# Kernel tuning notes

Hardware: AMD Instinct MI355X
Metric: run time of the kernel (lower is better)

The kernel has to match this reference:

```python
import jax, jax.numpy as jnp
import numpy as np
from jax import lax

B = 16
C_IN = 103      # image_channels / conv_inputs (spectral bands)
H = W = 9       # patch size
C_CONV = 256    # conv_outputs == primary_unit_size (in_size of routing)
N_PRIM = 32     # num_primary_units (in_units, contracted dim)
N_OUT = 103     # num_output_units
D_OUT = 16      # output_unit_size
N_ITER = 3
REC = H * W * C_IN          # 8343
H1 = int(REC * 2 / 3)       # 5562
H2 = int(REC * 3 / 2)       # 12514


def squash(s, axis):
    # torch: mag_sq/(1+mag_sq) * s/mag, reduced over `axis`
    mag_sq = jnp.sum(s * s, axis=axis, keepdims=True)
    mag = jnp.sqrt(mag_sq)
    return mag_sq / (1.0 + mag_sq) * (s / mag)


def setup_inputs() -> dict:
    key = jax.random.key(0)
    ks = jax.random.split(key, 10)
    x = jax.random.normal(ks[0], (B, C_IN, H, W), jnp.float32)
    conv_w = 0.05 * jax.random.normal(ks[1], (C_CONV, C_IN, 3, 3), jnp.float32)
    conv_b = jnp.zeros((C_CONV,), jnp.float32)
    # torch: nn.Parameter(torch.randn(1, in_size, out_units, out_size, in_units)); drop leading 1
    W_caps = jax.random.normal(ks[2], (C_CONV, N_OUT, D_OUT, N_PRIM), jnp.float32)
    fc1_w = 0.02 * jax.random.normal(ks[3], (N_OUT * D_OUT, H1), jnp.float32)
    fc1_b = jnp.zeros((H1,), jnp.float32)
    fc2_w = 0.02 * jax.random.normal(ks[4], (H1, H2), jnp.float32)
    fc2_b = jnp.zeros((H2,), jnp.float32)
    fc3_w = 0.02 * jax.random.normal(ks[5], (H2, REC), jnp.float32)
    fc3_b = jnp.zeros((REC,), jnp.float32)
    return {"x": x, "conv_w": conv_w, "conv_b": conv_b, "W_caps": W_caps,
            "fc1_w": fc1_w, "fc1_b": fc1_b, "fc2_w": fc2_w, "fc2_b": fc2_b,
            "fc3_w": fc3_w, "fc3_b": fc3_b}


def reference(x, conv_w, conv_b, W_caps, fc1_w, fc1_b, fc2_w, fc2_b, fc3_w, fc3_b):
    # ConvLayer: 3x3 valid conv + relu -> [B, C_CONV, 7, 7]
    h = lax.conv_general_dilated(x, conv_w, (1, 1), 'VALID',
                                 dimension_numbers=('NCHW', 'OIHW', 'NCHW'))
    h = jax.nn.relu(h + conv_b[None, :, None, None])

    # PrimaryCapsuleLayer: N_PRIM identical AdaptiveAvgPool2d(1) units
    p = h.mean(axis=(2, 3))                                   # [B, C_CONV]
    u = jnp.broadcast_to(p[:, None, :], (B, N_PRIM, C_CONV))  # [B, N_PRIM, C_CONV]
    u = squash(u, axis=2)

    # CapsuleLayer dynamic routing
    xt = u.transpose(0, 2, 1)                                 # [B, C_CONV, N_PRIM]
    # u_hat[b,c,j,o] = sum_i W[c,j,o,i] * xt[b,c,i]
    u_hat = jnp.einsum('cjoi,bci->bcjo', W_caps, xt)          # [B, C_CONV, N_OUT, D_OUT]

    b_ij = jnp.ones((1, C_CONV, N_OUT, 1), u_hat.dtype)
    v_j = None
    for _ in range(N_ITER):
        c_ij = jax.nn.softmax(b_ij, axis=1)                   # softmax over in_size
        s_j = jnp.sum(c_ij * u_hat, axis=1, keepdims=True)    # [B, 1, N_OUT, D_OUT]
        v_j = squash(s_j, axis=2)                             # torch squashes over out_units dim
        agree = jnp.sum(u_hat * v_j, axis=3, keepdims=True)   # [B, C_CONV, N_OUT, 1]
        b_ij = b_ij + agree.mean(axis=0, keepdims=True)

    v = v_j[:, 0]                                             # [B, N_OUT, D_OUT]
    # band_attention = ||v_j||_2 over out_size, shape [B, N_OUT, 1, 1] (torch)
    ba = jnp.linalg.norm(v, axis=-1, keepdims=True)[..., None]

    # ReconstructionLayer on attention-weighted capsules
    f = (v * ba[..., 0]).reshape(B, -1)                       # [B, N_OUT*D_OUT]
    f = f @ fc1_w + fc1_b
    f = f @ fc2_w + fc2_b
    f = f @ fc3_w + fc3_b
    recon = f.reshape(B, C_IN, H, W)
    return ba, recon
```

## Files before the change

kernel.cpp:

```cpp
#include <hip/hip_runtime.h>
#include <math.h>

#define BATCH 16
#define CIN 103
#define CCONV 256
#define NOUT 103
#define DOUT 16
#define RECSZ 8343
#define H1SZ 5562
#define H2SZ 12514

#define WS_P      0
#define WS_SQ     4096
#define WS_WSUM   8192
#define WS_BB     430080
#define WS_S      456448
#define WS_FACTOR 482816
#define WS_F0     483072
#define WS_F1     509440
#define WS_F2     598432

__global__ __launch_bounds__(256) void init_k(float* __restrict__ f1, const float* __restrict__ b1,
                                              float* __restrict__ f2, const float* __restrict__ b2,
                                              float* __restrict__ f3, const float* __restrict__ b3,
                                              float* __restrict__ bb) {
    int i = blockIdx.x * 256 + threadIdx.x;
    if (i < 16 * H1SZ) { f1[i] = b1[i % H1SZ]; return; }
    i -= 16 * H1SZ;
    if (i < 16 * H2SZ) { f2[i] = b2[i % H2SZ]; return; }
    i -= 16 * H2SZ;
    if (i < 16 * RECSZ) { f3[i] = b3[i % RECSZ]; return; }
    i -= 16 * RECSZ;
    if (i < 103 * 256) bb[i] = 1.0f;
}

__global__ __launch_bounds__(256) void conv_pool_k(const float* __restrict__ x,
                                                   const float* __restrict__ w,
                                                   const float* __restrict__ cb,
                                                   float* __restrict__ p) {
    int b = blockIdx.x >> 6;
    int cob = (blockIdx.x & 63) << 2;
    __shared__ float xs[CIN * 81];
    int t = threadIdx.x;
    for (int i = t; i < CIN * 81; i += 256) xs[i] = x[(size_t)b * CIN * 81 + i];
    __syncthreads();
    int wave = t >> 6, lane = t & 63;
    int co = cob + wave;
    co = __builtin_amdgcn_readfirstlane(co);
    int pos = lane < 49 ? lane : 0;
    int oh = pos / 7, ow = pos % 7;
    const float* wp = w + (size_t)co * CIN * 9;
    const float* xp = xs + oh * 9 + ow;
    float acc = 0.f;
    for (int ci = 0; ci < CIN; ++ci) {
#pragma unroll
        for (int kh = 0; kh < 3; ++kh)
#pragma unroll
            for (int kw = 0; kw < 3; ++kw)
                acc = fmaf(xp[ci * 81 + kh * 9 + kw], wp[ci * 9 + kh * 3 + kw], acc);
    }
    acc += cb[co];
    acc = fmaxf(acc, 0.f);
    if (lane >= 49) acc = 0.f;
#pragma unroll
    for (int off = 32; off; off >>= 1) acc += __shfl_down(acc, off);
    if (lane == 0) p[b * 256 + co] = acc * (1.0f / 49.0f);
}

__global__ __launch_bounds__(256) void squash_p_k(const float* __restrict__ p, float* __restrict__ sq) {
    int b = blockIdx.x, c = threadIdx.x;
    float v = p[b * 256 + c];
    float ss = v * v;
#pragma unroll
    for (int off = 32; off; off >>= 1) ss += __shfl_down(ss, off);
    __shared__ float red[4];
    if ((c & 63) == 0) red[c >> 6] = ss;
    __syncthreads();
    float ms = red[0] + red[1] + red[2] + red[3];
    float mag = sqrtf(ms);
    sq[b * 256 + c] = v * mag / (1.f + ms);
}

__global__ __launch_bounds__(256) void wsum_k(const float* __restrict__ Wc, float* __restrict__ wsum) {
    int idx = blockIdx.x * 256 + threadIdx.x;
    const float4* p4 = (const float4*)(Wc + (size_t)idx * 32);
    float s = 0.f;
#pragma unroll
    for (int q = 0; q < 8; ++q) { float4 v = p4[q]; s += v.x + v.y + v.z + v.w; }
    wsum[idx] = s;
}

__global__ __launch_bounds__(256) void route_s_k(const float* __restrict__ sq,
                                                 const float* __restrict__ wsum,
                                                 const float* __restrict__ bb,
                                                 float* __restrict__ s_out) {
    int j = blockIdx.x;
    int t = threadIdx.x;
    __shared__ float sqst[4096];
    __shared__ float wls[4096];
    __shared__ float cc[256];
    __shared__ float red[8];
    float bv = bb[j * 256 + t];
    for (int i = t; i < 4096; i += 256) {
        sqst[i] = sq[((i & 15) << 8) + (i >> 4)];
        wls[i] = wsum[(size_t)(i >> 4) * (103 * 16) + j * 16 + (i & 15)];
    }
    int wave = t >> 6, lane = t & 63;
    float m = bv;
#pragma unroll
    for (int off = 32; off; off >>= 1) m = fmaxf(m, __shfl_down(m, off));
    if (lane == 0) red[wave] = m;
    __syncthreads();
    m = fmaxf(fmaxf(red[0], red[1]), fmaxf(red[2], red[3]));
    float e = expf(bv - m);
    float ssum = e;
#pragma unroll
    for (int off = 32; off; off >>= 1) ssum += __shfl_down(ssum, off);
    if (lane == 0) red[4 + wave] = ssum;
    __syncthreads();
    ssum = red[4] + red[5] + red[6] + red[7];
    cc[t] = e / ssum;
    __syncthreads();
    for (int i = t; i < 4096; i += 256) sqst[i] *= cc[i >> 4];
    __syncthreads();
    int b = t >> 4, o = t & 15;
    float acc = 0.f;
    for (int c = 0; c < 256; ++c)
        acc = fmaf(sqst[c * 16 + b], wls[c * 16 + o], acc);
    s_out[((size_t)b * 103 + j) * 16 + o] = acc;
}

__global__ __launch_bounds__(256) void factor_k(const float* __restrict__ s, float* __restrict__ factor) {
    int t = threadIdx.x;
    int b = t >> 4, o = t & 15;
    float ms = 0.f;
    for (int j = 0; j < 103; ++j) {
        float v = s[((size_t)b * 103 + j) * 16 + o];
        ms = fmaf(v, v, ms);
    }
    factor[t] = sqrtf(ms) / (1.f + ms);
}

__global__ __launch_bounds__(256) void route_upd_k(const float* __restrict__ sq,
                                                   const float* __restrict__ wsum,
                                                   const float* __restrict__ s,
                                                   const float* __restrict__ factor,
                                                   float* __restrict__ bb) {
    int j = blockIdx.x;
    int t = threadIdx.x;
    __shared__ float vs[256];
    {
        int b = t >> 4, o = t & 15;
        vs[t] = s[((size_t)b * 103 + j) * 16 + o] * factor[t];
    }
    __syncthreads();
    const float4* wp = (const float4*)(wsum + ((size_t)t * 103 + j) * 16);
    float4 w0 = wp[0], w1 = wp[1], w2 = wp[2], w3 = wp[3];
    float wv[16] = {w0.x, w0.y, w0.z, w0.w, w1.x, w1.y, w1.z, w1.w,
                    w2.x, w2.y, w2.z, w2.w, w3.x, w3.y, w3.z, w3.w};
    float acc = 0.f;
#pragma unroll
    for (int b = 0; b < 16; ++b) {
        float d = 0.f;
#pragma unroll
        for (int o = 0; o < 16; ++o) d = fmaf(wv[o], vs[b * 16 + o], d);
        acc = fmaf(sq[b * 256 + t], d, acc);
    }
    bb[j * 256 + t] += acc * (1.0f / 16.0f);
}

__global__ __launch_bounds__(256) void final_v_k(const float* __restrict__ s,
                                                 const float* __restrict__ factor,
                                                 float* __restrict__ out_ba,
                                                 float* __restrict__ f0) {
    int idx = blockIdx.x * 256 + threadIdx.x;
    if (idx >= 16 * 103) return;
    int b = idx / 103;
    const float4* sp = (const float4*)(s + (size_t)idx * 16);
    float4 s0 = sp[0], s1 = sp[1], s2 = sp[2], s3 = sp[3];
    float sv[16] = {s0.x, s0.y, s0.z, s0.w, s1.x, s1.y, s1.z, s1.w,
                    s2.x, s2.y, s2.z, s2.w, s3.x, s3.y, s3.z, s3.w};
    float v[16];
    float nrm2 = 0.f;
#pragma unroll
    for (int o = 0; o < 16; ++o) {
        v[o] = sv[o] * factor[b * 16 + o];
        nrm2 = fmaf(v[o], v[o], nrm2);
    }
    float ba = sqrtf(nrm2);
    out_ba[idx] = ba;
    float4* fp = (float4*)(f0 + (size_t)idx * 16);
    float4 r0 = {v[0] * ba, v[1] * ba, v[2] * ba, v[3] * ba};
    float4 r1 = {v[4] * ba, v[5] * ba, v[6] * ba, v[7] * ba};
    float4 r2 = {v[8] * ba, v[9] * ba, v[10] * ba, v[11] * ba};
    float4 r3 = {v[12] * ba, v[13] * ba, v[14] * ba, v[15] * ba};
    fp[0] = r0; fp[1] = r1; fp[2] = r2; fp[3] = r3;
}

template <bool V2>
__global__ __launch_bounds__(256) void fc_k(const float* __restrict__ in,
                                            const float* __restrict__ w,
                                            float* __restrict__ out,
                                            int K, int N, int kchunk) {
    extern __shared__ float sact[];
    const int k0 = blockIdx.y * kchunk;
    int nk = K - k0; if (nk > kchunk) nk = kchunk;
    for (int i = threadIdx.x; i < (nk << 4); i += 256)
        sact[i] = in[(i & 15) * K + k0 + (i >> 4)];
    __syncthreads();

    const int c0 = blockIdx.x * 512 + (threadIdx.x << 1);
    const bool st0 = c0 < N;
    const bool st1 = c0 + 1 < N;
    const int c = st0 ? c0 : 0;
    const int off1 = st1 ? 1 : 0;
    const float* wp = w + (size_t)k0 * N + c;
    const size_t Ns = (size_t)N;

    float a0[16], a1[16];
#pragma unroll
    for (int b = 0; b < 16; ++b) { a0[b] = 0.f; a1[b] = 0.f; }

    int k = 0;
    for (; k + 4 <= nk; k += 4) {
        float w00, w01, w10, w11, w20, w21, w30, w31;
        if (V2) {
            float2 q0 = *(const float2*)(wp);
            float2 q1 = *(const float2*)(wp + Ns);
            float2 q2 = *(const float2*)(wp + 2 * Ns);
            float2 q3 = *(const float2*)(wp + 3 * Ns);
            w00 = q0.x; w01 = q0.y; w10 = q1.x; w11 = q1.y;
            w20 = q2.x; w21 = q2.y; w30 = q3.x; w31 = q3.y;
        } else {
            w00 = wp[0];          w01 = wp[off1];
            w10 = wp[Ns];         w11 = wp[Ns + off1];
            w20 = wp[2 * Ns];     w21 = wp[2 * Ns + off1];
            w30 = wp[3 * Ns];     w31 = wp[3 * Ns + off1];
        }
        wp += 4 * Ns;
        const float* s0 = sact + (k << 4);
#pragma unroll
        for (int b = 0; b < 16; ++b) {
            float v0 = s0[b], v1 = s0[16 + b], v2 = s0[32 + b], v3 = s0[48 + b];
            a0[b] = fmaf(v0, w00, a0[b]);
            a1[b] = fmaf(v0, w01, a1[b]);
            a0[b] = fmaf(v1, w10, a0[b]);
            a1[b] = fmaf(v1, w11, a1[b]);
            a0[b] = fmaf(v2, w20, a0[b]);
            a1[b] = fmaf(v2, w21, a1[b]);
            a0[b] = fmaf(v3, w30, a0[b]);
            a1[b] = fmaf(v3, w31, a1[b]);
        }
    }
    for (; k < nk; ++k) {
        float wv0, wv1;
        if (V2) { float2 q = *(const float2*)(wp); wv0 = q.x; wv1 = q.y; }
        else    { wv0 = wp[0]; wv1 = wp[off1]; }
        wp += Ns;
        const float* s0 = sact + (k << 4);
#pragma unroll
        for (int b = 0; b < 16; ++b) {
            a0[b] = fmaf(s0[b], wv0, a0[b]);
            a1[b] = fmaf(s0[b], wv1, a1[b]);
        }
    }
    if (st0) {
#pragma unroll
        for (int b = 0; b < 16; ++b) atomicAdd(&out[b * Ns + c], a0[b]);
    }
    if (st1) {
#pragma unroll
        for (int b = 0; b < 16; ++b) atomicAdd(&out[b * Ns + c + 1], a1[b]);
    }
}

extern "C" void kernel_launch(void* const* d_in, const int* in_sizes, int n_in,
                              void* d_out, int out_size, void* d_ws, size_t ws_size,
                              hipStream_t stream) {
    const float* x      = (const float*)d_in[0];
    const float* conv_w = (const float*)d_in[1];
    const float* conv_b = (const float*)d_in[2];
    const float* W_caps = (const float*)d_in[3];
    const float* fc1_w  = (const float*)d_in[4];
    const float* fc1_b  = (const float*)d_in[5];
    const float* fc2_w  = (const float*)d_in[6];
    const float* fc2_b  = (const float*)d_in[7];
    const float* fc3_w  = (const float*)d_in[8];
    const float* fc3_b  = (const float*)d_in[9];
    float* out = (float*)d_out;
    float* ws  = (float*)d_ws;

    float* p      = ws + WS_P;
    float* sq     = ws + WS_SQ;
    float* wsum   = ws + WS_WSUM;
    float* bb     = ws + WS_BB;
    float* s      = ws + WS_S;
    float* factor = ws + WS_FACTOR;
    float* f0     = ws + WS_F0;
    float* f1     = ws + WS_F1;
    float* f2     = ws + WS_F2;
    float* ba_out = out;
    float* recon  = out + 1648;

    init_k<<<1755, 256, 0, stream>>>(f1, fc1_b, f2, fc2_b, recon, fc3_b, bb);

    conv_pool_k<<<1024, 256, 0, stream>>>(x, conv_w, conv_b, p);
    squash_p_k<<<16, 256, 0, stream>>>(p, sq);
    wsum_k<<<1648, 256, 0, stream>>>(W_caps, wsum);

    for (int it = 0; it < 3; ++it) {
        route_s_k<<<103, 256, 0, stream>>>(sq, wsum, bb, s);
        factor_k<<<1, 256, 0, stream>>>(s, factor);
        if (it < 2)
            route_upd_k<<<103, 256, 0, stream>>>(sq, wsum, s, factor, bb);
    }
    final_v_k<<<7, 256, 0, stream>>>(s, factor, ba_out, f0);

    fc_k<true><<<dim3(11, 46), 256, 36 * 16 * 4, stream>>>(f0, fc1_w, f1, 1648, H1SZ, 36);
    fc_k<true><<<dim3(25, 20), 256, 279 * 16 * 4, stream>>>(f1, fc2_w, f2, H1SZ, H2SZ, 279);
    fc_k<false><<<dim3(17, 30), 256, 418 * 16 * 4, stream>>>(f2, fc3_w, recon, H2SZ, RECSZ, 418);
}
```

Measured before the change: 1.071 ms.

## Replace atomic split-K with partial buffers, transposed activations, and double-buffered weight loads

The three FC layers now write per-K-chunk partial sums to workspace, and separate reduction kernels sum them and add the bias. This removes the atomicAdd traffic and the bias-init kernel. Activations are kept in a k-major transposed layout, so shared-memory staging reads contiguously. The inner loop loads weights in groups of 8 rows with register double buffering to hide global load latency. The grids are re-split to use more K chunks and occupancy is raised with launch bounds, at the cost of extra partial-buffer memory traffic and three more launches.

```diff
diff --git a/kernel.cpp b/kernel.cpp
--- a/kernel.cpp
+++ b/kernel.cpp
@@ -19,18 +19,12 @@
 #define WS_F0     483072
 #define WS_F1     509440
 #define WS_F2     598432
-
-__global__ __launch_bounds__(256) void init_k(float* __restrict__ f1, const float* __restrict__ b1,
-                                              float* __restrict__ f2, const float* __restrict__ b2,
-                                              float* __restrict__ f3, const float* __restrict__ b3,
-                                              float* __restrict__ bb) {
+#define WS_PART1  798656
+#define WS_PART2  4536320
+#define WS_PART3  12345056
+
+__global__ __launch_bounds__(256) void init_bb_k(float* __restrict__ bb) {
     int i = blockIdx.x * 256 + threadIdx.x;
-    if (i < 16 * H1SZ) { f1[i] = b1[i % H1SZ]; return; }
-    i -= 16 * H1SZ;
-    if (i < 16 * H2SZ) { f2[i] = b2[i % H2SZ]; return; }
-    i -= 16 * H2SZ;
-    if (i < 16 * RECSZ) { f3[i] = b3[i % RECSZ]; return; }
-    i -= 16 * RECSZ;
     if (i < 103 * 256) bb[i] = 1.0f;
 }
 
@@ -172,10 +166,11 @@
 __global__ __launch_bounds__(256) void final_v_k(const float* __restrict__ s,
                                                  const float* __restrict__ factor,
                                                  float* __restrict__ out_ba,
-                                                 float* __restrict__ f0) {
+                                                 float* __restrict__ f0t) {
     int idx = blockIdx.x * 256 + threadIdx.x;
     if (idx >= 16 * 103) return;
     int b = idx / 103;
+    int j = idx - b * 103;
     const float4* sp = (const float4*)(s + (size_t)idx * 16);
     float4 s0 = sp[0], s1 = sp[1], s2 = sp[2], s3 = sp[3];
     float sv[16] = {s0.x, s0.y, s0.z, s0.w, s1.x, s1.y, s1.z, s1.w,
@@ -189,24 +184,53 @@
     }
     float ba = sqrtf(nrm2);
     out_ba[idx] = ba;
-    float4* fp = (float4*)(f0 + (size_t)idx * 16);
-    float4 r0 = {v[0] * ba, v[1] * ba, v[2] * ba, v[3] * ba};
-    float4 r1 = {v[4] * ba, v[5] * ba, v[6] * ba, v[7] * ba};
-    float4 r2 = {v[8] * ba, v[9] * ba, v[10] * ba, v[11] * ba};
-    float4 r3 = {v[12] * ba, v[13] * ba, v[14] * ba, v[15] * ba};
-    fp[0] = r0; fp[1] = r1; fp[2] = r2; fp[3] = r3;
-}
-
-template <bool V2>
-__global__ __launch_bounds__(256) void fc_k(const float* __restrict__ in,
-                                            const float* __restrict__ w,
-                                            float* __restrict__ out,
-                                            int K, int N, int kchunk) {
+    float* fp = f0t + ((size_t)j << 8) + b;
+#pragma unroll
+    for (int o = 0; o < 16; ++o) fp[o << 4] = v[o] * ba;
+}
+
+#define FC_LOADG(b0, b1, kk)                                          \
+    {                                                                 \
+        const float* wq = wp + (size_t)(kk) * Ns;                     \
+        if (V2) {                                                     \
+            _Pragma("unroll")                                         \
+            for (int r = 0; r < 8; ++r) {                             \
+                float2 q = *(const float2*)(wq + (size_t)r * Ns);     \
+                b0[r] = q.x; b1[r] = q.y;                             \
+            }                                                         \
+        } else {                                                      \
+            _Pragma("unroll")                                         \
+            for (int r = 0; r < 8; ++r) {                             \
+                b0[r] = wq[(size_t)r * Ns];                           \
+                b1[r] = wq[(size_t)r * Ns + off1];                    \
+            }                                                         \
+        }                                                             \
+    }
+
+#define FC_COMP(b0, b1, kk)                                           \
+    {                                                                 \
+        _Pragma("unroll")                                             \
+        for (int r = 0; r < 8; ++r) {                                 \
+            const float* s0 = sact + (((kk) + r) << 4);               \
+            _Pragma("unroll")                                         \
+            for (int bq = 0; bq < 16; ++bq) {                         \
+                float v = s0[bq];                                     \
+                a0[bq] = fmaf(v, b0[r], a0[bq]);                      \
+                a1[bq] = fmaf(v, b1[r], a1[bq]);                      \
+            }                                                         \
+        }                                                             \
+    }
+
+template <bool V2, bool OUT_T>
+__global__ __launch_bounds__(256, 4) void fc_k(const float* __restrict__ in,
+                                               const float* __restrict__ w,
+                                               float* __restrict__ part,
+                                               int K, int N, int kchunk) {
     extern __shared__ float sact[];
     const int k0 = blockIdx.y * kchunk;
     int nk = K - k0; if (nk > kchunk) nk = kchunk;
     for (int i = threadIdx.x; i < (nk << 4); i += 256)
-        sact[i] = in[(i & 15) * K + k0 + (i >> 4)];
+        sact[i] = in[((size_t)k0 << 4) + i];
     __syncthreads();
 
     const int c0 = blockIdx.x * 512 + (threadIdx.x << 1);
@@ -222,41 +246,26 @@
     for (int b = 0; b < 16; ++b) { a0[b] = 0.f; a1[b] = 0.f; }
 
     int k = 0;
-    for (; k + 4 <= nk; k += 4) {
-        float w00, w01, w10, w11, w20, w21, w30, w31;
-        if (V2) {
-            float2 q0 = *(const float2*)(wp);
-            float2 q1 = *(const float2*)(wp + Ns);
-            float2 q2 = *(const float2*)(wp + 2 * Ns);
-            float2 q3 = *(const float2*)(wp + 3 * Ns);
-            w00 = q0.x; w01 = q0.y; w10 = q1.x; w11 = q1.y;
-            w20 = q2.x; w21 = q2.y; w30 = q3.x; w31 = q3.y;
-        } else {
-            w00 = wp[0];          w01 = wp[off1];
-            w10 = wp[Ns];         w11 = wp[Ns + off1];
-            w20 = wp[2 * Ns];     w21 = wp[2 * Ns + off1];
-            w30 = wp[3 * Ns];     w31 = wp[3 * Ns + off1];
-        }
-        wp += 4 * Ns;
-        const float* s0 = sact + (k << 4);
-#pragma unroll
-        for (int b = 0; b < 16; ++b) {
-            float v0 = s0[b], v1 = s0[16 + b], v2 = s0[32 + b], v3 = s0[48 + b];
-            a0[b] = fmaf(v0, w00, a0[b]);
-            a1[b] = fmaf(v0, w01, a1[b]);
-            a0[b] = fmaf(v1, w10, a0[b]);
-            a1[b] = fmaf(v1, w11, a1[b]);
-            a0[b] = fmaf(v2, w20, a0[b]);
-            a1[b] = fmaf(v2, w21, a1[b]);
-            a0[b] = fmaf(v3, w30, a0[b]);
-            a1[b] = fmaf(v3, w31, a1[b]);
+    {
+        const int ng = nk >> 3;
+        if (ng > 0) {
+            float A0[8], A1[8], B0[8], B1[8];
+            FC_LOADG(A0, A1, 0);
+            int g = 0;
+            for (; g + 2 <= ng; g += 2) {
+                FC_LOADG(B0, B1, (g + 1) << 3);
+                FC_COMP(A0, A1, g << 3);
+                if (g + 2 < ng) FC_LOADG(A0, A1, (g + 2) << 3);
+                FC_COMP(B0, B1, (g + 1) << 3);
+            }
+            if (g < ng) FC_COMP(A0, A1, g << 3);
+            k = ng << 3;
         }
     }
     for (; k < nk; ++k) {
         float wv0, wv1;
-        if (V2) { float2 q = *(const float2*)(wp); wv0 = q.x; wv1 = q.y; }
-        else    { wv0 = wp[0]; wv1 = wp[off1]; }
-        wp += Ns;
+        if (V2) { float2 q = *(const float2*)(wp + (size_t)k * Ns); wv0 = q.x; wv1 = q.y; }
+        else    { wv0 = wp[(size_t)k * Ns]; wv1 = wp[(size_t)k * Ns + off1]; }
         const float* s0 = sact + (k << 4);
 #pragma unroll
         for (int b = 0; b < 16; ++b) {
@@ -264,14 +273,42 @@
             a1[b] = fmaf(s0[b], wv1, a1[b]);
         }
     }
-    if (st0) {
-#pragma unroll
-        for (int b = 0; b < 16; ++b) atomicAdd(&out[b * Ns + c], a0[b]);
-    }
-    if (st1) {
-#pragma unroll
-        for (int b = 0; b < 16; ++b) atomicAdd(&out[b * Ns + c + 1], a1[b]);
-    }
+
+    float* po = part + (size_t)blockIdx.y * (Ns << 4);
+    if (OUT_T) {
+        if (st0) {
+            float* q = po + ((size_t)c << 4);
+#pragma unroll
+            for (int b = 0; b < 16; ++b) q[b] = a0[b];
+        }
+        if (st1) {
+            float* q = po + ((size_t)(c + 1) << 4);
+#pragma unroll
+            for (int b = 0; b < 16; ++b) q[b] = a1[b];
+        }
+    } else {
+        if (st0) {
+#pragma unroll
+            for (int b = 0; b < 16; ++b) po[(size_t)b * Ns + c] = a0[b];
+        }
+        if (st1) {
+#pragma unroll
+            for (int b = 0; b < 16; ++b) po[(size_t)b * Ns + c + 1] = a1[b];
+        }
+    }
+}
+
+template <bool T>
+__global__ __launch_bounds__(256) void fcred_k(const float* __restrict__ P,
+                                               const float* __restrict__ bias,
+                                               float* __restrict__ out,
+                                               int total, int ny, int N) {
+    int i = blockIdx.x * 256 + threadIdx.x;
+    if (i >= total) return;
+    float sv = T ? bias[i >> 4] : bias[i % N];
+    const float* p = P + i;
+    for (int y = 0; y < ny; ++y) sv += p[(size_t)y * total];
+    out[i] = sv;
 }
 
 extern "C" void kernel_launch(void* const* d_in, const int* in_sizes, int n_in,
@@ -299,10 +336,13 @@
     float* f0     = ws + WS_F0;
     float* f1     = ws + WS_F1;
     float* f2     = ws + WS_F2;
+    float* part1  = ws + WS_PART1;
+    float* part2  = ws + WS_PART2;
+    float* part3  = ws + WS_PART3;
     float* ba_out = out;
     float* recon  = out + 1648;
 
-    init_k<<<1755, 256, 0, stream>>>(f1, fc1_b, f2, fc2_b, recon, fc3_b, bb);
+    init_bb_k<<<103, 256, 0, stream>>>(bb);
 
     conv_pool_k<<<1024, 256, 0, stream>>>(x, conv_w, conv_b, p);
     squash_p_k<<<16, 256, 0, stream>>>(p, sq);
@@ -316,7 +356,12 @@
     }
     final_v_k<<<7, 256, 0, stream>>>(s, factor, ba_out, f0);
 
-    fc_k<true><<<dim3(11, 46), 256, 36 * 16 * 4, stream>>>(f0, fc1_w, f1, 1648, H1SZ, 36);
-    fc_k<true><<<dim3(25, 20), 256, 279 * 16 * 4, stream>>>(f1, fc2_w, f2, H1SZ, H2SZ, 279);
-    fc_k<false><<<dim3(17, 30), 256, 418 * 16 * 4, stream>>>(f2, fc3_w, recon, H2SZ, RECSZ, 418);
-}
+    fc_k<true, true><<<dim3(11, 42), 256, 40 * 64, stream>>>(f0, fc1_w, part1, 1648, H1SZ, 40);
+    fcred_k<true><<<348, 256, 0, stream>>>(part1, fc1_b, f1, 16 * H1SZ, 42, H1SZ);
+
+    fc_k<true, true><<<dim3(25, 39), 256, 144 * 64, stream>>>(f1, fc2_w, part2, H1SZ, H2SZ, 144);
+    fcred_k<true><<<783, 256, 0, stream>>>(part2, fc2_b, f2, 16 * H2SZ, 39, H2SZ);
+
+    fc_k<false, false><<<dim3(17, 61), 256, 208 * 64, stream>>>(f2, fc3_w, part3, H2SZ, RECSZ, 208);
+    fcred_k<false><<<522, 256, 0, stream>>>(part3, fc3_b, recon, 16 * RECSZ, 61, RECSZ);
+}
```

Result: slower. 2.174 ms (+103.0%).

## Replace atomic split-K accumulation with partial buffers and reduction kernels

Applied to the files above, without the earlier changes.

The FC layers no longer atomically add split-K partial sums into bias-initialized outputs. Each K-chunk now writes its own partial buffer, and a separate reduction kernel sums the chunks and adds the bias. Intermediate activations are stored transposed (k-major, batch-minor) so the shared-memory activation load is contiguous. The K-split counts are increased for more parallelism, at the cost of extra workspace traffic and three additional reduction launches.

```diff
diff --git a/kernel.cpp b/kernel.cpp
--- a/kernel.cpp
+++ b/kernel.cpp
@@ -19,18 +19,12 @@
 #define WS_F0     483072
 #define WS_F1     509440
 #define WS_F2     598432
-
-__global__ __launch_bounds__(256) void init_k(float* __restrict__ f1, const float* __restrict__ b1,
-                                              float* __restrict__ f2, const float* __restrict__ b2,
-                                              float* __restrict__ f3, const float* __restrict__ b3,
-                                              float* __restrict__ bb) {
+#define WS_PART1  798656
+#define WS_PART2  4536320
+#define WS_PART3  12345056
+
+__global__ __launch_bounds__(256) void init_bb_k(float* __restrict__ bb) {
     int i = blockIdx.x * 256 + threadIdx.x;
-    if (i < 16 * H1SZ) { f1[i] = b1[i % H1SZ]; return; }
-    i -= 16 * H1SZ;
-    if (i < 16 * H2SZ) { f2[i] = b2[i % H2SZ]; return; }
-    i -= 16 * H2SZ;
-    if (i < 16 * RECSZ) { f3[i] = b3[i % RECSZ]; return; }
-    i -= 16 * RECSZ;
     if (i < 103 * 256) bb[i] = 1.0f;
 }
 
@@ -172,10 +166,11 @@
 __global__ __launch_bounds__(256) void final_v_k(const float* __restrict__ s,
                                                  const float* __restrict__ factor,
                                                  float* __restrict__ out_ba,
-                                                 float* __restrict__ f0) {
+                                                 float* __restrict__ f0t) {
     int idx = blockIdx.x * 256 + threadIdx.x;
     if (idx >= 16 * 103) return;
     int b = idx / 103;
+    int j = idx - b * 103;
     const float4* sp = (const float4*)(s + (size_t)idx * 16);
     float4 s0 = sp[0], s1 = sp[1], s2 = sp[2], s3 = sp[3];
     float sv[16] = {s0.x, s0.y, s0.z, s0.w, s1.x, s1.y, s1.z, s1.w,
@@ -189,24 +184,21 @@
     }
     float ba = sqrtf(nrm2);
     out_ba[idx] = ba;
-    float4* fp = (float4*)(f0 + (size_t)idx * 16);
-    float4 r0 = {v[0] * ba, v[1] * ba, v[2] * ba, v[3] * ba};
-    float4 r1 = {v[4] * ba, v[5] * ba, v[6] * ba, v[7] * ba};
-    float4 r2 = {v[8] * ba, v[9] * ba, v[10] * ba, v[11] * ba};
-    float4 r3 = {v[12] * ba, v[13] * ba, v[14] * ba, v[15] * ba};
-    fp[0] = r0; fp[1] = r1; fp[2] = r2; fp[3] = r3;
-}
-
-template <bool V2>
+    float* fp = f0t + ((size_t)j << 8) + b;
+#pragma unroll
+    for (int o = 0; o < 16; ++o) fp[o << 4] = v[o] * ba;
+}
+
+template <bool V2, bool OUT_T>
 __global__ __launch_bounds__(256) void fc_k(const float* __restrict__ in,
                                             const float* __restrict__ w,
-                                            float* __restrict__ out,
+                                            float* __restrict__ part,
                                             int K, int N, int kchunk) {
     extern __shared__ float sact[];
     const int k0 = blockIdx.y * kchunk;
     int nk = K - k0; if (nk > kchunk) nk = kchunk;
     for (int i = threadIdx.x; i < (nk << 4); i += 256)
-        sact[i] = in[(i & 15) * K + k0 + (i >> 4)];
+        sact[i] = in[((size_t)k0 << 4) + i];
     __syncthreads();
 
     const int c0 = blockIdx.x * 512 + (threadIdx.x << 1);
@@ -264,14 +256,42 @@
             a1[b] = fmaf(s0[b], wv1, a1[b]);
         }
     }
-    if (st0) {
-#pragma unroll
-        for (int b = 0; b < 16; ++b) atomicAdd(&out[b * Ns + c], a0[b]);
-    }
-    if (st1) {
-#pragma unroll
-        for (int b = 0; b < 16; ++b) atomicAdd(&out[b * Ns + c + 1], a1[b]);
-    }
+
+    float* po = part + (size_t)blockIdx.y * (Ns << 4);
+    if (OUT_T) {
+        if (st0) {
+            float* q = po + ((size_t)c << 4);
+#pragma unroll
+            for (int b = 0; b < 16; ++b) q[b] = a0[b];
+        }
+        if (st1) {
+            float* q = po + ((size_t)(c + 1) << 4);
+#pragma unroll
+            for (int b = 0; b < 16; ++b) q[b] = a1[b];
+        }
+    } else {
+        if (st0) {
+#pragma unroll
+            for (int b = 0; b < 16; ++b) po[(size_t)b * Ns + c] = a0[b];
+        }
+        if (st1) {
+#pragma unroll
+            for (int b = 0; b < 16; ++b) po[(size_t)b * Ns + c + 1] = a1[b];
+        }
+    }
+}
+
+template <bool T>
+__global__ __launch_bounds__(256) void fcred_k(const float* __restrict__ P,
+                                               const float* __restrict__ bias,
+                                               float* __restrict__ out,
+                                               int total, int ny, int N) {
+    int i = blockIdx.x * 256 + threadIdx.x;
+    if (i >= total) return;
+    float sv = T ? bias[i >> 4] : bias[i % N];
+    const float* p = P + i;
+    for (int y = 0; y < ny; ++y) sv += p[(size_t)y * total];
+    out[i] = sv;
 }
 
 extern "C" void kernel_launch(void* const* d_in, const int* in_sizes, int n_in,
@@ -299,10 +319,13 @@
     float* f0     = ws + WS_F0;
     float* f1     = ws + WS_F1;
     float* f2     = ws + WS_F2;
+    float* part1  = ws + WS_PART1;
+    float* part2  = ws + WS_PART2;
+    float* part3  = ws + WS_PART3;
     float* ba_out = out;
     float* recon  = out + 1648;
 
-    init_k<<<1755, 256, 0, stream>>>(f1, fc1_b, f2, fc2_b, recon, fc3_b, bb);
+    init_bb_k<<<103, 256, 0, stream>>>(bb);
 
     conv_pool_k<<<1024, 256, 0, stream>>>(x, conv_w, conv_b, p);
     squash_p_k<<<16, 256, 0, stream>>>(p, sq);
@@ -316,7 +339,12 @@
     }
     final_v_k<<<7, 256, 0, stream>>>(s, factor, ba_out, f0);
 
-    fc_k<true><<<dim3(11, 46), 256, 36 * 16 * 4, stream>>>(f0, fc1_w, f1, 1648, H1SZ, 36);
-    fc_k<true><<<dim3(25, 20), 256, 279 * 16 * 4, stream>>>(f1, fc2_w, f2, H1SZ, H2SZ, 279);
-    fc_k<false><<<dim3(17, 30), 256, 418 * 16 * 4, stream>>>(f2, fc3_w, recon, H2SZ, RECSZ, 418);
-}
+    fc_k<true, true><<<dim3(11, 42), 256, 40 * 64, stream>>>(f0, fc1_w, part1, 1648, H1SZ, 40);
+    fcred_k<true><<<348, 256, 0, stream>>>(part1, fc1_b, f1, 16 * H1SZ, 42, H1SZ);
+
+    fc_k<true, true><<<dim3(25, 39), 256, 144 * 64, stream>>>(f1, fc2_w, part2, H1SZ, H2SZ, 144);
+    fcred_k<true><<<783, 256, 0, stream>>>(part2, fc2_b, f2, 16 * H2SZ, 39, H2SZ);
+
+    fc_k<false, false><<<dim3(17, 61), 256, 208 * 64, stream>>>(f2, fc3_w, part3, H2SZ, RECSZ, 208);
+    fcred_k<false><<<522, 256, 0, stream>>>(part3, fc3_b, recon, 16 * RECSZ, 61, RECSZ);
+}
```

Result: faster. 986.2 us (-7.9%).
